# Kernel optimization log

Measured on AMD Instinct MI355X. Metric: run time of the kernel, lower is better.

The kernel has to match this reference:

```python
import jax, jax.numpy as jnp
import numpy as np

B, T, N, D = 8, 12, 325, 256
H = 8
HD = D // H
FF = 1024
SCALE = HD ** -0.5
EPS = 1e-5
NEG_INF = jnp.float32(-1e30)


def layernorm(x, w, b):
    mu = jnp.mean(x, axis=-1, keepdims=True)
    var = jnp.mean(jnp.square(x - mu), axis=-1, keepdims=True)
    return (x - mu) * jax.lax.rsqrt(var + EPS) * w + b


def mha(x, wq, bq, wk, bk, wv, bv, wo, bo, mask):
    # x: (G, L, D); mask: (L, L) bool, True = keep, or None
    G, L, _ = x.shape
    q = (x @ wq + bq).reshape(G, L, H, HD)
    k = (x @ wk + bk).reshape(G, L, H, HD)
    v = (x @ wv + bv).reshape(G, L, H, HD)
    scores = jnp.einsum('glhd,gmhd->ghlm', q, k) * SCALE
    if mask is not None:
        scores = jnp.where(mask[None, None], scores, NEG_INF)
    attn = jax.nn.softmax(scores, axis=-1)
    out = jnp.einsum('ghlm,gmhd->glhd', attn, v).reshape(G, L, D)
    return out @ wo + bo


def setup_inputs() -> dict:
    key = jax.random.key(0)
    ks = jax.random.split(key, 16)
    s = 0.02
    inp = {
        'x': jax.random.normal(ks[0], (B, T, N, D), jnp.float32),
        'adj_mask': jax.random.randint(ks[1], (N, N), 0, 2, jnp.int32),
        'sa_wq': jax.random.normal(ks[2], (D, D)) * s, 'sa_bq': jnp.zeros((D,)),
        'sa_wk': jax.random.normal(ks[3], (D, D)) * s, 'sa_bk': jnp.zeros((D,)),
        'sa_wv': jax.random.normal(ks[4], (D, D)) * s, 'sa_bv': jnp.zeros((D,)),
        'sa_wo': jax.random.normal(ks[5], (D, D)) * s, 'sa_bo': jnp.zeros((D,)),
        'sa_ln_w': jnp.ones((D,)), 'sa_ln_b': jnp.zeros((D,)),
        'ta_wq': jax.random.normal(ks[6], (D, D)) * s, 'ta_bq': jnp.zeros((D,)),
        'ta_wk': jax.random.normal(ks[7], (D, D)) * s, 'ta_bk': jnp.zeros((D,)),
        'ta_wv': jax.random.normal(ks[8], (D, D)) * s, 'ta_bv': jnp.zeros((D,)),
        'ta_wo': jax.random.normal(ks[9], (D, D)) * s, 'ta_bo': jnp.zeros((D,)),
        'ta_ln_w': jnp.ones((D,)), 'ta_ln_b': jnp.zeros((D,)),
        'f_w1': jax.random.normal(ks[10], (D, FF)) * s, 'f_b1': jnp.zeros((FF,)),
        'f_w2': jax.random.normal(ks[11], (FF, D)) * s, 'f_b2': jnp.zeros((D,)),
        'f_ln_w': jnp.ones((D,)), 'f_ln_b': jnp.zeros((D,)),
    }
    return inp


def reference(x, adj_mask,
              sa_wq, sa_bq, sa_wk, sa_bk, sa_wv, sa_bv, sa_wo, sa_bo, sa_ln_w, sa_ln_b,
              ta_wq, ta_bq, ta_wk, ta_bk, ta_wv, ta_bv, ta_wo, ta_bo, ta_ln_w, ta_ln_b,
              f_w1, f_b1, f_w2, f_b2, f_ln_w, f_ln_b):
    # Spatial attention over N at each (b, t)
    xs = x.reshape(B * T, N, D)
    sa = mha(xs, sa_wq, sa_bq, sa_wk, sa_bk, sa_wv, sa_bv, sa_wo, sa_bo,
             adj_mask != 0).reshape(B, T, N, D)
    x = layernorm(x + sa, sa_ln_w, sa_ln_b)

    # Temporal attention over T at each (b, n), causal
    xt = x.transpose(0, 2, 1, 3).reshape(B * N, T, D)
    causal = jnp.tril(jnp.ones((T, T), dtype=bool))
    ta = mha(xt, ta_wq, ta_bq, ta_wk, ta_bk, ta_wv, ta_bv, ta_wo, ta_bo, causal)
    ta = ta.reshape(B, N, T, D).transpose(0, 2, 1, 3)
    x = layernorm(x + ta, ta_ln_w, ta_ln_b)

    # FFN with exact GELU (torch nn.GELU default)
    h = jax.nn.gelu(x @ f_w1 + f_b1, approximate=False)
    out = layernorm(x + (h @ f_w2 + f_b2), f_ln_w, f_ln_b)
    return out
```

## Files before the change

kernel.cpp:

```cpp
#include <hip/hip_runtime.h>
#include <hip/hip_bf16.h>
#include <math.h>

#define B_   8
#define T_   12
#define NN   325
#define DD   256
#define HH   8
#define HD   32
#define FFD  1024
#define MTOK (B_*T_*NN)
#define QKVD 768
#define ATT_SCALE 0.17677669529663687f
#define LN_EPS 1e-5f
#define MROWS 336

typedef __attribute__((ext_vector_type(8))) __bf16 bf16x8;
typedef __attribute__((ext_vector_type(4))) float  f32x4;
typedef __attribute__((ext_vector_type(4))) short  shortx4;
typedef __attribute__((ext_vector_type(8))) unsigned short ushortx8;

static __device__ inline float bf2f(unsigned short u) {
  union { float f; unsigned int i; } c; c.i = ((unsigned int)u) << 16; return c.f;
}

#if __has_builtin(__builtin_amdgcn_mfma_f32_16x16x16bf16_1k)
#define MFMA16(a,b,c) __builtin_amdgcn_mfma_f32_16x16x16bf16_1k((a),(b),(c),0,0,0)
#else
static __device__ inline f32x4 mfma16_fn(shortx4 a, shortx4 b, f32x4 c) {
  f32x4 d;
  asm volatile("v_mfma_f32_16x16x16_bf16 %0, %1, %2, %3"
               : "=v"(d) : "v"(a), "v"(b), "v"(c));
  return d;
}
#define MFMA16(a,b,c) mfma16_fn((a),(b),(c))
#endif

__global__ __launch_bounds__(256) void gemm_strip2(
    const __hip_bfloat16* __restrict__ A,
    const __hip_bfloat16* __restrict__ Wt,
    const float* __restrict__ bias,
    __hip_bfloat16* __restrict__ Cb,
    int Mr, int Nr, int Kr, int gelu)
{
  constexpr int BP = 136;
  __shared__ __hip_bfloat16 Bs[128 * BP];

  const int NS  = Nr >> 7;
  const int nwg = gridDim.x;
  const int orig = blockIdx.x;
  const int qq = nwg >> 3, rr = nwg & 7;
  const int xcd = orig & 7, off = orig >> 3;
  const int id = (xcd < rr ? xcd * (qq + 1) : rr * (qq + 1) + (xcd - rr) * qq) + off;
  const int n0 = (id % NS) * 128;
  const int mg = id / NS;

  const int tid = threadIdx.x;
  const int w = tid >> 6, lane = tid & 63;
  const int lr = lane & 15, lg = lane >> 4;
  const int KC = Kr >> 7;

  float bv[8];
  #pragma unroll
  for (int j = 0; j < 8; ++j) bv[j] = bias[n0 + j * 16 + lr];

  const int strip0 = mg * 128 + w * 32;
  int ar0 = strip0 + lr;      if (ar0 >= Mr) ar0 = Mr - 1;
  int ar1 = strip0 + 16 + lr; if (ar1 >= Mr) ar1 = Mr - 1;

  f32x4 acc0[8] = {}, acc1[8] = {};

  for (int kc = 0; kc < KC; ++kc) {
    if (kc) __syncthreads();
    for (int u = tid; u < 128 * 16; u += 256) {
      int row = u >> 4, c8 = (u & 15) * 8;
      *(bf16x8*)&Bs[row * BP + c8] =
          *(const bf16x8*)&Wt[(size_t)(n0 + row) * Kr + kc * 128 + c8];
    }
    __syncthreads();

    const __hip_bfloat16* a0p = A + (size_t)ar0 * Kr + kc * 128 + lg * 8;
    const __hip_bfloat16* a1p = A + (size_t)ar1 * Kr + kc * 128 + lg * 8;
    bf16x8 a0[4], a1[4];
    #pragma unroll
    for (int k = 0; k < 4; ++k) {
      a0[k] = *(const bf16x8*)(a0p + k * 32);
      a1[k] = *(const bf16x8*)(a1p + k * 32);
    }
    #pragma unroll
    for (int k = 0; k < 4; ++k)
      #pragma unroll
      for (int j = 0; j < 8; ++j) {
        bf16x8 bfr = *(const bf16x8*)&Bs[(j * 16 + lr) * BP + k * 32 + lg * 8];
        acc0[j] = __builtin_amdgcn_mfma_f32_16x16x32_bf16(a0[k], bfr, acc0[j], 0, 0, 0);
        acc1[j] = __builtin_amdgcn_mfma_f32_16x16x32_bf16(a1[k], bfr, acc1[j], 0, 0, 0);
      }
  }

  #pragma unroll
  for (int j = 0; j < 8; ++j) {
    int col = n0 + j * 16 + lr;
    #pragma unroll
    for (int q = 0; q < 4; ++q) {
      int g0 = strip0 + lg * 4 + q;
      if (g0 < Mr) {
        float c = acc0[j][q] + bv[j];
        if (gelu) c = 0.5f * c * (1.f + erff(c * 0.70710678118654752f));
        Cb[(size_t)g0 * Nr + col] = __float2bfloat16(c);
      }
      int g1 = strip0 + 16 + lg * 4 + q;
      if (g1 < Mr) {
        float c = acc1[j][q] + bv[j];
        if (gelu) c = 0.5f * c * (1.f + erff(c * 0.70710678118654752f));
        Cb[(size_t)g1 * Nr + col] = __float2bfloat16(c);
      }
    }
  }
}

struct PrepPtrs {
  const float* w[10];
  const float* b[6];
};

__global__ __launch_bounds__(256) void prep_all(
    PrepPtrs p, const int* __restrict__ adj, const float* __restrict__ x0,
    __hip_bfloat16* __restrict__ Wb, float* __restrict__ qkvb ,
    float* __restrict__ maskf, __hip_bfloat16* __restrict__ x0b)
{
  __shared__ float t[32][33];
  const int z = blockIdx.z;

  if (z < 10) {
    const int Kz = (z == 9) ? 1024 : 256;
    const int Nz = (z == 8) ? 1024 : 256;
    if ((int)blockIdx.x >= Nz / 32 || (int)blockIdx.y >= Kz / 32) return;
    static const unsigned int dsto[10] = {0, 65536, 131072, 196608, 262144,
                                          327680, 393216, 458752, 524288, 786432};
    const float scale = (z == 0 || z == 3) ? ATT_SCALE : 1.f;
    const float* W = p.w[z];
    __hip_bfloat16* Wt = Wb + dsto[z];
    const int n0 = blockIdx.x * 32, k0 = blockIdx.y * 32;
    const int tx = threadIdx.x & 31, ty = threadIdx.x >> 5;
    #pragma unroll
    for (int i = 0; i < 32; i += 8)
      t[ty + i][tx] = W[(size_t)(k0 + ty + i) * Nz + n0 + tx];
    __syncthreads();
    #pragma unroll
    for (int i = 0; i < 32; i += 8)
      Wt[(size_t)(n0 + ty + i) * Kz + k0 + tx] = __float2bfloat16(t[tx][ty + i] * scale);
    return;
  }

  const int bx = blockIdx.x + blockIdx.y * 32;
  const int gid = bx * 256 + threadIdx.x;

  if (z == 10) {
    if (gid < 1536) {
      int i = gid & 767;
      int which = gid < 768 ? 0 : 1;
      int sub = i >> 8, j = i & 255;
      float v = p.b[which * 3 + sub][j];
      if (sub == 0) v *= ATT_SCALE;
      qkvb[which * 768 + i] = v;
    } else if (gid < 1536 + NN * MROWS) {
      int idx = gid - 1536;
      int l = idx / MROWS, m = idx % MROWS;
      float v;
      if (m >= NN) v = -INFINITY;
      else v = (adj[l * NN + m] != 0) ? 0.f : -1e30f;
      maskf[idx] = v;
    }
    return;
  }

  const int n4 = MTOK * DD / 4;
  for (int i = gid; i < n4; i += 262144) {
    float4 v = reinterpret_cast<const float4*>(x0)[i];
    union { shortx4 s; __hip_bfloat16 h[4]; } u;
    u.h[0] = __float2bfloat16(v.x); u.h[1] = __float2bfloat16(v.y);
    u.h[2] = __float2bfloat16(v.z); u.h[3] = __float2bfloat16(v.w);
    reinterpret_cast<shortx4*>(x0b)[i] = u.s;
  }
}

__global__ __launch_bounds__(256) void spatial_attn_mfma(
    const __hip_bfloat16* __restrict__ qkv,
    const float* __restrict__ maskf,
    __hip_bfloat16* __restrict__ out)
{
  constexpr int KP = 40;
  constexpr int VP = 340;
  __shared__ unsigned short Kl[MROWS * KP];
  __shared__ unsigned short Vt[32 * VP];

  const int g = blockIdx.x, h = blockIdx.y;
  const int tid = threadIdx.x;
  const int w = tid >> 6, lane = tid & 63;
  const int lq = lane & 15, lg = lane >> 4;

  const size_t baseQ = (size_t)g * NN * QKVD + (size_t)h * HD;
  const size_t baseK = baseQ + 256;
  const size_t baseV = baseQ + 512;

  for (int idx = tid; idx < 32 * (VP - NN); idx += 256) {
    int d = idx / (VP - NN), kk = NN + idx % (VP - NN);
    Vt[d * VP + kk] = 0;
  }
  for (int idx = tid; idx < (MROWS - NN) * KP; idx += 256)
    Kl[NN * KP + idx] = 0;
  for (int idx = tid; idx < NN * 4; idx += 256) {
    int row = idx >> 2, cc = (idx & 3) * 8;
    union { bf16x8 v; unsigned short u[8]; } kv, vv;
    kv.v = *(const bf16x8*)&qkv[baseK + (size_t)row * QKVD + cc];
    *(bf16x8*)&Kl[row * KP + cc] = kv.v;
    vv.v = *(const bf16x8*)&qkv[baseV + (size_t)row * QKVD + cc];
    #pragma unroll
    for (int j = 0; j < 8; ++j) Vt[(cc + j) * VP + row] = vv.u[j];
  }
  __syncthreads();

  for (int qt = w; qt < 21; qt += 4) {
    const int query = qt * 16 + lq;
    const int qc = query < NN ? query : NN - 1;
    const bf16x8 qf = *(const bf16x8*)&qkv[baseQ + (size_t)qc * QKVD + lg * 8];
    const float* mrow = maskf + (size_t)qc * MROWS;

    float lmax = -INFINITY;
    #pragma unroll
    for (int t = 0; t < 21; ++t) {
      bf16x8 kf = *(const bf16x8*)&Kl[(t * 16 + lq) * KP + lg * 8];
      f32x4 st = __builtin_amdgcn_mfma_f32_16x16x32_bf16(
          kf, qf, (f32x4){0.f, 0.f, 0.f, 0.f}, 0, 0, 0);
      const int kbase = t * 16 + lg * 4;
      float4 mb = *(const float4*)&mrow[kbase];
      lmax = fmaxf(lmax, fmaxf(fmaxf(st[0] + mb.x, st[1] + mb.y),
                               fmaxf(st[2] + mb.z, st[3] + mb.w)));
    }
    lmax = fmaxf(lmax, __shfl_xor(lmax, 16));
    lmax = fmaxf(lmax, __shfl_xor(lmax, 32));

    f32x4 accL = {0.f, 0.f, 0.f, 0.f};
    f32x4 accH = {0.f, 0.f, 0.f, 0.f};
    float lsum = 0.f;
    #pragma unroll
    for (int t = 0; t < 21; ++t) {
      bf16x8 kf = *(const bf16x8*)&Kl[(t * 16 + lq) * KP + lg * 8];
      f32x4 st = __builtin_amdgcn_mfma_f32_16x16x32_bf16(
          kf, qf, (f32x4){0.f, 0.f, 0.f, 0.f}, 0, 0, 0);
      const int kbase = t * 16 + lg * 4;
      float4 mb = *(const float4*)&mrow[kbase];
      float p0 = __expf(st[0] + mb.x - lmax);
      float p1 = __expf(st[1] + mb.y - lmax);
      float p2 = __expf(st[2] + mb.z - lmax);
      float p3 = __expf(st[3] + mb.w - lmax);
      lsum += (p0 + p1) + (p2 + p3);
      union { shortx4 s4; __hip_bfloat16 hh[4]; } up;
      up.hh[0] = __float2bfloat16(p0); up.hh[1] = __float2bfloat16(p1);
      up.hh[2] = __float2bfloat16(p2); up.hh[3] = __float2bfloat16(p3);
      shortx4 vaL = *(const shortx4*)&Vt[lq * VP + kbase];
      shortx4 vaH = *(const shortx4*)&Vt[(lq + 16) * VP + kbase];
      accL = MFMA16(vaL, up.s4, accL);
      accH = MFMA16(vaH, up.s4, accH);
    }
    lsum += __shfl_xor(lsum, 16);
    lsum += __shfl_xor(lsum, 32);

    if (query < NN) {
      const float inv = 1.f / lsum;
      const size_t ob = ((size_t)(g * NN + query)) * DD + (size_t)h * HD;
      union { shortx4 s4; __hip_bfloat16 hh[4]; } uL, uH;
      #pragma unroll
      for (int q = 0; q < 4; ++q) {
        uL.hh[q] = __float2bfloat16(accL[q] * inv);
        uH.hh[q] = __float2bfloat16(accH[q] * inv);
      }
      *(shortx4*)&out[ob + lg * 4]      = uL.s4;
      *(shortx4*)&out[ob + 16 + lg * 4] = uH.s4;
    }
  }
}

__global__ __launch_bounds__(256) void temporal_attn(
    const __hip_bfloat16* __restrict__ qkv, __hip_bfloat16* __restrict__ out)
{
  int idx = blockIdx.x * 256 + threadIdx.x;
  const int total = B_ * NN * HH * T_;
  if (idx >= total) return;

  int t  = idx % T_;
  int h  = (idx / T_) % HH;
  int n  = (idx / (T_ * HH)) % NN;
  int b  = idx / (T_ * HH * NN);

  const size_t tq = (size_t)((b * T_ + t) * NN + n) * QKVD + h * HD;
  float qr[HD];
  #pragma unroll
  for (int c8 = 0; c8 < 4; ++c8) {
    ushortx8 u = *(const ushortx8*)&qkv[tq + c8 * 8];
    #pragma unroll
    for (int j = 0; j < 8; ++j) qr[c8 * 8 + j] = bf2f(u[j]);
  }

  float o[HD] = {};
  float mrun = -INFINITY, lrun = 0.f;

  for (int tt = 0; tt <= t; ++tt) {
    const size_t tk = (size_t)((b * T_ + tt) * NN + n) * QKVD + h * HD;
    float s = 0.f;
    #pragma unroll
    for (int c8 = 0; c8 < 4; ++c8) {
      ushortx8 u = *(const ushortx8*)&qkv[tk + 256 + c8 * 8];
      #pragma unroll
      for (int j = 0; j < 8; ++j) s += qr[c8 * 8 + j] * bf2f(u[j]);
    }
    float mnew = fmaxf(mrun, s);
    float corr = __expf(mrun - mnew);
    float p = __expf(s - mnew);
    lrun = lrun * corr + p;
    #pragma unroll
    for (int c8 = 0; c8 < 4; ++c8) {
      ushortx8 u = *(const ushortx8*)&qkv[tk + 512 + c8 * 8];
      #pragma unroll
      for (int j = 0; j < 8; ++j) o[c8 * 8 + j] = o[c8 * 8 + j] * corr + p * bf2f(u[j]);
    }
    mrun = mnew;
  }

  float inv = 1.f / lrun;
  __hip_bfloat16* op = out + ((size_t)((b * T_ + t) * NN + n)) * DD + h * HD;
  #pragma unroll
  for (int d0 = 0; d0 < HD; d0 += 4) {
    union { shortx4 s; __hip_bfloat16 h4[4]; } u;
    #pragma unroll
    for (int j = 0; j < 4; ++j) u.h4[j] = __float2bfloat16(o[d0 + j] * inv);
    *reinterpret_cast<shortx4*>(op + d0) = u.s;
  }
}

__global__ __launch_bounds__(64) void add_ln(
    const float* __restrict__ x, const __hip_bfloat16* __restrict__ r,
    const float* __restrict__ w, const float* __restrict__ bb,
    float* __restrict__ y, __hip_bfloat16* __restrict__ ybf)
{
  const size_t row = blockIdx.x;
  const int lane = threadIdx.x;

  const float4 xv = reinterpret_cast<const float4*>(x + row * DD)[lane];
  union { shortx4 s4; unsigned short u[4]; } rv;
  rv.s4 = reinterpret_cast<const shortx4*>(r + row * DD)[lane];
  float e[4] = {xv.x + bf2f(rv.u[0]), xv.y + bf2f(rv.u[1]),
                xv.z + bf2f(rv.u[2]), xv.w + bf2f(rv.u[3])};

  float s  = e[0] + e[1] + e[2] + e[3];
  float ss = e[0]*e[0] + e[1]*e[1] + e[2]*e[2] + e[3]*e[3];
  #pragma unroll
  for (int off = 32; off > 0; off >>= 1) {
    s  += __shfl_xor(s,  off, 64);
    ss += __shfl_xor(ss, off, 64);
  }
  float mu  = s * (1.f / DD);
  float var = ss * (1.f / DD) - mu * mu;
  float rs  = rsqrtf(var + LN_EPS);

  const float4 wv = reinterpret_cast<const float4*>(w)[lane];
  const float4 bv = reinterpret_cast<const float4*>(bb)[lane];
  float o0 = (e[0] - mu) * rs * wv.x + bv.x;
  float o1 = (e[1] - mu) * rs * wv.y + bv.y;
  float o2 = (e[2] - mu) * rs * wv.z + bv.z;
  float o3 = (e[3] - mu) * rs * wv.w + bv.w;
  float4 yv = {o0, o1, o2, o3};
  reinterpret_cast<float4*>(y + row * DD)[lane] = yv;
  if (ybf) {
    union { shortx4 s4; __hip_bfloat16 h4[4]; } u;
    u.h4[0] = __float2bfloat16(o0); u.h4[1] = __float2bfloat16(o1);
    u.h4[2] = __float2bfloat16(o2); u.h4[3] = __float2bfloat16(o3);
    reinterpret_cast<shortx4*>(ybf + row * DD)[lane] = u.s4;
  }
}

extern "C" void kernel_launch(void* const* d_in, const int* in_sizes, int n_in,
                              void* d_out, int out_size, void* d_ws, size_t ws_size,
                              hipStream_t stream)
{
  const float* x0   = (const float*)d_in[0];
  const int*   adj  = (const int*)  d_in[1];
  const float* sa_wq = (const float*)d_in[2];
  const float* sa_bq = (const float*)d_in[3];
  const float* sa_wk = (const float*)d_in[4];
  const float* sa_bk = (const float*)d_in[5];
  const float* sa_wv = (const float*)d_in[6];
  const float* sa_bv = (const float*)d_in[7];
  const float* sa_wo = (const float*)d_in[8];
  const float* sa_bo = (const float*)d_in[9];
  const float* sa_lw = (const float*)d_in[10];
  const float* sa_lb = (const float*)d_in[11];
  const float* ta_wq = (const float*)d_in[12];
  const float* ta_bq = (const float*)d_in[13];
  const float* ta_wk = (const float*)d_in[14];
  const float* ta_bk = (const float*)d_in[15];
  const float* ta_wv = (const float*)d_in[16];
  const float* ta_bv = (const float*)d_in[17];
  const float* ta_wo = (const float*)d_in[18];
  const float* ta_bo = (const float*)d_in[19];
  const float* ta_lw = (const float*)d_in[20];
  const float* ta_lb = (const float*)d_in[21];
  const float* f_w1  = (const float*)d_in[22];
  const float* f_b1  = (const float*)d_in[23];
  const float* f_w2  = (const float*)d_in[24];
  const float* f_b2  = (const float*)d_in[25];
  const float* f_lw  = (const float*)d_in[26];
  const float* f_lb  = (const float*)d_in[27];

  float* out = (float*)d_out;
  float* ws  = (float*)d_ws;

  const size_t P = (size_t)MTOK * DD;
  if (ws_size < 7 * P * sizeof(float)) return;

  float* R0 = ws;
  __hip_bfloat16* QKVb = (__hip_bfloat16*)(ws + P);
  __hip_bfloat16* HIDb = (__hip_bfloat16*)(ws + P);
  __hip_bfloat16* PRJ  = (__hip_bfloat16*)(ws + 3 * P);
  float* R4 = ws + 4 * P;
  __hip_bfloat16* X0b  = (__hip_bfloat16*)(ws + 5 * P);
  __hip_bfloat16* X1b  = (__hip_bfloat16*)(ws + 5 * P + P / 2);
  __hip_bfloat16* ATTb = (__hip_bfloat16*)(ws + 6 * P);
  __hip_bfloat16* Wb   = (__hip_bfloat16*)(ws + 6 * P + P / 2);

  __hip_bfloat16* sa_qkv_t = Wb;
  __hip_bfloat16* ta_qkv_t = Wb + 196608;
  __hip_bfloat16* sa_wo_t  = Wb + 393216;
  __hip_bfloat16* ta_wo_t  = Wb + 458752;
  __hip_bfloat16* f_w1_t   = Wb + 524288;
  __hip_bfloat16* f_w2_t   = Wb + 786432;
  float* qkvb  = (float*)(Wb + 1048576);
  float* maskf = qkvb + 1536;

  PrepPtrs pp;
  pp.w[0] = sa_wq; pp.w[1] = sa_wk; pp.w[2] = sa_wv;
  pp.w[3] = ta_wq; pp.w[4] = ta_wk; pp.w[5] = ta_wv;
  pp.w[6] = sa_wo; pp.w[7] = ta_wo; pp.w[8] = f_w1; pp.w[9] = f_w2;
  pp.b[0] = sa_bq; pp.b[1] = sa_bk; pp.b[2] = sa_bv;
  pp.b[3] = ta_bq; pp.b[4] = ta_bk; pp.b[5] = ta_bv;
  prep_all<<<dim3(32, 32, 12), 256, 0, stream>>>(pp, adj, x0, Wb, qkvb, maskf, X0b);

  const int MG = (MTOK + 127) / 128;
  auto gemmS = [&](const __hip_bfloat16* A, const __hip_bfloat16* Wt, const float* bias,
                   __hip_bfloat16* Cb, int Nr, int Kr, int gelu) {
    int nwg = (Nr / 128) * MG;
    gemm_strip2<<<nwg, 256, 0, stream>>>(A, Wt, bias, Cb, MTOK, Nr, Kr, gelu);
  };

  gemmS(X0b, sa_qkv_t, qkvb, QKVb, QKVD, DD, 0);
  spatial_attn_mfma<<<dim3(B_ * T_, HH), 256, 0, stream>>>(QKVb, maskf, ATTb);
  gemmS(ATTb, sa_wo_t, sa_bo, PRJ, DD, DD, 0);
  add_ln<<<MTOK, 64, 0, stream>>>(x0, PRJ, sa_lw, sa_lb, R4, X1b);

  gemmS(X1b, ta_qkv_t, qkvb + 768, QKVb, QKVD, DD, 0);
  {
    int total = B_ * NN * HH * T_;
    temporal_attn<<<(total + 255) / 256, 256, 0, stream>>>(QKVb, ATTb);
  }
  gemmS(ATTb, ta_wo_t, ta_bo, PRJ, DD, DD, 0);
  add_ln<<<MTOK, 64, 0, stream>>>(R4, PRJ, ta_lw, ta_lb, R0, X0b);

  gemmS(X0b, f_w1_t, f_b1, HIDb, FFD, DD, 1);
  gemmS(HIDb, f_w2_t, f_b2, PRJ, DD, FFD, 0);
  add_ln<<<MTOK, 64, 0, stream>>>(R0, PRJ, f_lw, f_lb, out, nullptr);
}
```

Before: 422.1 us.

## Use single-pass online softmax in spatial attention, processing two query tiles per wave

Replaces the two-pass softmax in the spatial attention kernel (one pass for the max, a second that recomputes QK^T for exp and PV) with a single-pass online softmax that rescales the running accumulators at every key tile. Each wave also handles two query tiles at once, so each K and V fragment read from LDS is reused and there is more independent MFMA work to interleave. This removes the duplicated QK MFMAs and mask loads. In exchange it adds per-tile cross-lane shuffles for the max, extra exp calls for the rescale factors, and more live registers.

```diff
diff --git a/kernel.cpp b/kernel.cpp
--- a/kernel.cpp
+++ b/kernel.cpp
@@ -125,7 +125,7 @@
 
 __global__ __launch_bounds__(256) void prep_all(
     PrepPtrs p, const int* __restrict__ adj, const float* __restrict__ x0,
-    __hip_bfloat16* __restrict__ Wb, float* __restrict__ qkvb ,
+    __hip_bfloat16* __restrict__ Wb, float* __restrict__ qkvb,
     float* __restrict__ maskf, __hip_bfloat16* __restrict__ x0b)
 {
   __shared__ float t[32][33];
@@ -220,60 +220,100 @@
   }
   __syncthreads();
 
-  for (int qt = w; qt < 21; qt += 4) {
-    const int query = qt * 16 + lq;
-    const int qc = query < NN ? query : NN - 1;
-    const bf16x8 qf = *(const bf16x8*)&qkv[baseQ + (size_t)qc * QKVD + lg * 8];
-    const float* mrow = maskf + (size_t)qc * MROWS;
-
-    float lmax = -INFINITY;
+  #pragma unroll 1
+  for (int i = 0; i < 3; ++i) {
+    const int qtA = w + 8 * i;
+    int qtB = qtA + 4;
+    const bool hasB = (qtB < 21);
+    if (!hasB) qtB = qtA;
+
+    const int queryA = qtA * 16 + lq;
+    const int queryB = qtB * 16 + lq;
+    const int qcB = queryB < NN ? queryB : NN - 1;
+    const bf16x8 qfA = *(const bf16x8*)&qkv[baseQ + (size_t)queryA * QKVD + lg * 8];
+    const bf16x8 qfB = *(const bf16x8*)&qkv[baseQ + (size_t)qcB * QKVD + lg * 8];
+    const float* mrowA = maskf + (size_t)queryA * MROWS;
+    const float* mrowB = maskf + (size_t)qcB * MROWS;
+
+    f32x4 accLA = {0.f,0.f,0.f,0.f}, accHA = {0.f,0.f,0.f,0.f};
+    f32x4 accLB = {0.f,0.f,0.f,0.f}, accHB = {0.f,0.f,0.f,0.f};
+    float mrunA = -INFINITY, lrunA = 0.f;
+    float mrunB = -INFINITY, lrunB = 0.f;
+
     #pragma unroll
     for (int t = 0; t < 21; ++t) {
+      const int kbase = t * 16 + lg * 4;
       bf16x8 kf = *(const bf16x8*)&Kl[(t * 16 + lq) * KP + lg * 8];
-      f32x4 st = __builtin_amdgcn_mfma_f32_16x16x32_bf16(
-          kf, qf, (f32x4){0.f, 0.f, 0.f, 0.f}, 0, 0, 0);
-      const int kbase = t * 16 + lg * 4;
-      float4 mb = *(const float4*)&mrow[kbase];
-      lmax = fmaxf(lmax, fmaxf(fmaxf(st[0] + mb.x, st[1] + mb.y),
-                               fmaxf(st[2] + mb.z, st[3] + mb.w)));
-    }
-    lmax = fmaxf(lmax, __shfl_xor(lmax, 16));
-    lmax = fmaxf(lmax, __shfl_xor(lmax, 32));
-
-    f32x4 accL = {0.f, 0.f, 0.f, 0.f};
-    f32x4 accH = {0.f, 0.f, 0.f, 0.f};
-    float lsum = 0.f;
-    #pragma unroll
-    for (int t = 0; t < 21; ++t) {
-      bf16x8 kf = *(const bf16x8*)&Kl[(t * 16 + lq) * KP + lg * 8];
-      f32x4 st = __builtin_amdgcn_mfma_f32_16x16x32_bf16(
-          kf, qf, (f32x4){0.f, 0.f, 0.f, 0.f}, 0, 0, 0);
-      const int kbase = t * 16 + lg * 4;
-      float4 mb = *(const float4*)&mrow[kbase];
-      float p0 = __expf(st[0] + mb.x - lmax);
-      float p1 = __expf(st[1] + mb.y - lmax);
-      float p2 = __expf(st[2] + mb.z - lmax);
-      float p3 = __expf(st[3] + mb.w - lmax);
-      lsum += (p0 + p1) + (p2 + p3);
-      union { shortx4 s4; __hip_bfloat16 hh[4]; } up;
-      up.hh[0] = __float2bfloat16(p0); up.hh[1] = __float2bfloat16(p1);
-      up.hh[2] = __float2bfloat16(p2); up.hh[3] = __float2bfloat16(p3);
+      f32x4 stA = __builtin_amdgcn_mfma_f32_16x16x32_bf16(
+          kf, qfA, (f32x4){0.f,0.f,0.f,0.f}, 0, 0, 0);
+      f32x4 stB = __builtin_amdgcn_mfma_f32_16x16x32_bf16(
+          kf, qfB, (f32x4){0.f,0.f,0.f,0.f}, 0, 0, 0);
+      float4 mbA = *(const float4*)&mrowA[kbase];
+      float4 mbB = *(const float4*)&mrowB[kbase];
+      float sA0 = stA[0]+mbA.x, sA1 = stA[1]+mbA.y, sA2 = stA[2]+mbA.z, sA3 = stA[3]+mbA.w;
+      float sB0 = stB[0]+mbB.x, sB1 = stB[1]+mbB.y, sB2 = stB[2]+mbB.z, sB3 = stB[3]+mbB.w;
+
+      float tA = fmaxf(fmaxf(sA0, sA1), fmaxf(sA2, sA3));
+      float tB = fmaxf(fmaxf(sB0, sB1), fmaxf(sB2, sB3));
+      tA = fmaxf(tA, __shfl_xor(tA, 16));
+      tB = fmaxf(tB, __shfl_xor(tB, 16));
+      tA = fmaxf(tA, __shfl_xor(tA, 32));
+      tB = fmaxf(tB, __shfl_xor(tB, 32));
+
+      const float mnA = fmaxf(mrunA, tA);
+      const float mnB = fmaxf(mrunB, tB);
+      const float cA = __expf(mrunA - mnA);
+      const float cB = __expf(mrunB - mnB);
+      mrunA = mnA; mrunB = mnB;
+
+      float pA0 = __expf(sA0 - mnA), pA1 = __expf(sA1 - mnA);
+      float pA2 = __expf(sA2 - mnA), pA3 = __expf(sA3 - mnA);
+      float pB0 = __expf(sB0 - mnB), pB1 = __expf(sB1 - mnB);
+      float pB2 = __expf(sB2 - mnB), pB3 = __expf(sB3 - mnB);
+      lrunA = lrunA * cA + ((pA0 + pA1) + (pA2 + pA3));
+      lrunB = lrunB * cB + ((pB0 + pB1) + (pB2 + pB3));
+
+      accLA *= cA; accHA *= cA; accLB *= cB; accHB *= cB;
+
+      union { shortx4 s4; __hip_bfloat16 hh[4]; } upA, upB;
+      upA.hh[0] = __float2bfloat16(pA0); upA.hh[1] = __float2bfloat16(pA1);
+      upA.hh[2] = __float2bfloat16(pA2); upA.hh[3] = __float2bfloat16(pA3);
+      upB.hh[0] = __float2bfloat16(pB0); upB.hh[1] = __float2bfloat16(pB1);
+      upB.hh[2] = __float2bfloat16(pB2); upB.hh[3] = __float2bfloat16(pB3);
+
       shortx4 vaL = *(const shortx4*)&Vt[lq * VP + kbase];
       shortx4 vaH = *(const shortx4*)&Vt[(lq + 16) * VP + kbase];
-      accL = MFMA16(vaL, up.s4, accL);
-      accH = MFMA16(vaH, up.s4, accH);
-    }
-    lsum += __shfl_xor(lsum, 16);
-    lsum += __shfl_xor(lsum, 32);
-
-    if (query < NN) {
-      const float inv = 1.f / lsum;
-      const size_t ob = ((size_t)(g * NN + query)) * DD + (size_t)h * HD;
+      accLA = MFMA16(vaL, upA.s4, accLA);
+      accHA = MFMA16(vaH, upA.s4, accHA);
+      accLB = MFMA16(vaL, upB.s4, accLB);
+      accHB = MFMA16(vaH, upB.s4, accHB);
+    }
+
+    lrunA += __shfl_xor(lrunA, 16);
+    lrunA += __shfl_xor(lrunA, 32);
+    lrunB += __shfl_xor(lrunB, 16);
+    lrunB += __shfl_xor(lrunB, 32);
+
+    {
+      const float inv = 1.f / lrunA;
+      const size_t ob = ((size_t)(g * NN + queryA)) * DD + (size_t)h * HD;
       union { shortx4 s4; __hip_bfloat16 hh[4]; } uL, uH;
       #pragma unroll
       for (int q = 0; q < 4; ++q) {
-        uL.hh[q] = __float2bfloat16(accL[q] * inv);
-        uH.hh[q] = __float2bfloat16(accH[q] * inv);
+        uL.hh[q] = __float2bfloat16(accLA[q] * inv);
+        uH.hh[q] = __float2bfloat16(accHA[q] * inv);
+      }
+      *(shortx4*)&out[ob + lg * 4]      = uL.s4;
+      *(shortx4*)&out[ob + 16 + lg * 4] = uH.s4;
+    }
+    if (hasB && queryB < NN) {
+      const float inv = 1.f / lrunB;
+      const size_t ob = ((size_t)(g * NN + queryB)) * DD + (size_t)h * HD;
+      union { shortx4 s4; __hip_bfloat16 hh[4]; } uL, uH;
+      #pragma unroll
+      for (int q = 0; q < 4; ++q) {
+        uL.hh[q] = __float2bfloat16(accLB[q] * inv);
+        uH.hh[q] = __float2bfloat16(accHB[q] * inv);
       }
       *(shortx4*)&out[ob + lg * 4]      = uL.s4;
       *(shortx4*)&out[ob + 16 + lg * 4] = uH.s4;
```

Result: faster. 412.8 us (-2.2%).
